# Performance work log

Hardware: AMD Instinct MI355X
Metric: run time of the kernel (lower is better)

The kernel has to match this reference:

```python
import jax, jax.numpy as jnp
import numpy as np

B_, L, D_MODEL = 2, 2048, 1024
EXPAND, D_INNER, D_STATE, DT_RANK, D_CONV = 2, 2048, 16, 64, 4
DT_MIN, DT_MAX = 0.001, 0.1


def setup_inputs() -> dict:
    key = jax.random.key(0)
    ks = jax.random.split(key, 8)
    s = lambda fan: 1.0 / np.sqrt(fan)
    # S4D-real style init for A: A = -exp(A_log), A_log = log(1..n) repeated over d_inner
    A0 = jnp.broadcast_to(jnp.arange(1, D_STATE + 1, dtype=jnp.float32), (D_INNER, D_STATE))
    return {
        "x": jax.random.normal(ks[0], (B_, L, D_MODEL), jnp.float32),
        "W_in": jax.random.normal(ks[1], (D_MODEL, 2 * D_INNER), jnp.float32) * s(D_MODEL),
        "conv_k": jax.random.normal(ks[2], (D_CONV, D_INNER // EXPAND, D_INNER), jnp.float32) * s(D_CONV * D_INNER // EXPAND),
        "conv_b": jnp.zeros((D_INNER,), jnp.float32),
        "W_x": jax.random.normal(ks[3], (D_INNER, DT_RANK + 2 * D_STATE), jnp.float32) * s(D_INNER),
        "W_dt": jax.random.normal(ks[4], (DT_RANK, D_INNER), jnp.float32) * s(DT_RANK),
        "b_dt": jnp.zeros((D_INNER,), jnp.float32),
        "A_log": jnp.log(A0),
        "D": jnp.ones((D_INNER,), jnp.float32),
        "W_out": jax.random.normal(ks[5], (D_INNER, D_MODEL), jnp.float32) * s(D_INNER),
    }


def reference(x, W_in, conv_k, conv_b, W_x, W_dt, b_dt, A_log, D, W_out):
    # in_proj -> split into ssm branch and gating residual branch
    xz = x @ W_in                                   # (b, l, 2*d_inner)
    xs, res = jnp.split(xz, 2, axis=-1)
    # causal grouped conv1d (feature_group_count = expand)
    xc = jax.lax.conv_general_dilated(
        xs, conv_k, window_strides=(1,), padding=[(D_CONV - 1, 0)],
        dimension_numbers=("NWC", "WIO", "NWC"), feature_group_count=EXPAND,
    ) + conv_b
    u = jax.nn.silu(xc)                             # (b, l, d_inner)
    # x_proj -> delta(low-rank), B, C
    dbc = u @ W_x                                   # (b, l, dt_rank + 2n)
    dt_raw = dbc[..., :DT_RANK]
    Bm = dbc[..., DT_RANK:DT_RANK + D_STATE]        # (b, l, n)
    Cm = dbc[..., DT_RANK + D_STATE:]               # (b, l, n)
    delta = jax.nn.softplus(dt_raw @ W_dt + b_dt)   # (b, l, d_inner)
    delta = jnp.clip(delta, DT_MIN, DT_MAX)
    A = -jnp.exp(A_log)                             # (d_inner, n)
    dA = jnp.exp(delta[..., None] * A)              # (b, l, d_inner, n)
    dBu = delta[..., None] * u[..., None] * Bm[:, :, None, :]  # (b, l, d_inner, n)

    def step(h, inp):
        dA_t, dBu_t, C_t = inp                      # (b,d,n),(b,d,n),(b,n)
        h = dA_t * h + dBu_t
        y_t = jnp.einsum('bdn,bn->bd', h, C_t)
        return h, y_t

    h0 = jnp.zeros((x.shape[0], D_INNER, D_STATE), dA.dtype)
    _, y = jax.lax.scan(step, h0, (dA.transpose(1, 0, 2, 3), dBu.transpose(1, 0, 2, 3), Cm.transpose(1, 0, 2)))
    y = y.transpose(1, 0, 2) + u * D                # (b, l, d_inner)
    out = (y * jax.nn.silu(res)) @ W_out            # (b, l, d_model)
    return out
```

## Files before the change

kernel.cpp:

```cpp
#include <hip/hip_runtime.h>
#include <math.h>


typedef unsigned short ushort_t;
typedef unsigned int uint_t;
typedef __bf16 bf16x8 __attribute__((ext_vector_type(8)));
typedef float floatx4 __attribute__((ext_vector_type(4)));

#define LDS_STRIDE 40

__device__ __forceinline__ float silu_f(float x) { return x / (1.0f + __expf(-x)); }

__device__ __forceinline__ unsigned short f2bf(float f) {
    unsigned u = __float_as_uint(f);
    unsigned r = u + 0x7fffu + ((u >> 16) & 1u);
    return (unsigned short)(r >> 16);
}
__device__ __forceinline__ float bf2f(unsigned short h) {
    return __uint_as_float(((unsigned)h) << 16);
}
__device__ __forceinline__ uint_t packhl(float v) {
    const unsigned short h = f2bf(v);
    const unsigned short l = f2bf(v - bf2f(h));
    return (uint_t)h | ((uint_t)l << 16);
}
__device__ __forceinline__ float unpack_sum(uint_t pk) {
    return __uint_as_float(pk << 16) + __uint_as_float(pk & 0xffff0000u);
}
__device__ __forceinline__ void unpack8(uint4 w0, uint4 w1, uint4& H, uint4& L) {
    H.x = (w0.x & 0xffffu) | (w0.y << 16);  L.x = (w0.x >> 16) | (w0.y & 0xffff0000u);
    H.y = (w0.z & 0xffffu) | (w0.w << 16);  L.y = (w0.z >> 16) | (w0.w & 0xffff0000u);
    H.z = (w1.x & 0xffffu) | (w1.y << 16);  L.z = (w1.x >> 16) | (w1.y & 0xffff0000u);
    H.w = (w1.z & 0xffffu) | (w1.w << 16);  L.w = (w1.z >> 16) | (w1.w & 0xffff0000u);
}

__global__ __launch_bounds__(256) void prep_all(
    const float* __restrict__ x, const float* __restrict__ W_in,
    const float* __restrict__ conv_k, const float* __restrict__ W_out,
    const float* __restrict__ W_x,
    uint_t* __restrict__ xpk,
    ushort_t* __restrict__ WinT_h, ushort_t* __restrict__ convkT_h,
    ushort_t* __restrict__ WoutT_h, ushort_t* __restrict__ WxT_h,
    ushort_t* __restrict__ XSP_h)
{
    __shared__ float ts[32][33];
    const int bid = blockIdx.x;
    const int t = threadIdx.x;
    if (bid < 4096) {
        const size_t i4 = ((size_t)bid * 256 + t) * 4;
        float4 v = *(const float4*)&x[i4];
        uint4 pk;
        pk.x = packhl(v.x); pk.y = packhl(v.y); pk.z = packhl(v.z); pk.w = packhl(v.w);
        *(uint4*)&xpk[i4] = pk;
        return;
    }
    if (bid >= 18432 && bid < 19456) {
        const int idx = (bid - 18432) * 256 + t;
        const int r = idx >> 11, k = idx & 2047;
        float v = (r < 96) ? W_x[(size_t)k * 96 + r] : 0.f;
        WxT_h[idx] = f2bf(v);
        return;
    }
    if (bid >= 19456) {
        const int idx = (bid - 19456) * 256 + t;
        const int b = idx / 6144, rem = idx % 6144;
        const int lp = rem >> 11, c = rem & 2047;
        XSP_h[((size_t)b * 2051 + lp) * 2048 + c] = 0;
        return;
    }
    const float* src; int R, C; ushort_t* dst; int bx, by;
    if (bid < 8192)       { src = W_in;   R = 1024; C = 4096; dst = WinT_h;
                            int l = bid - 4096;  bx = l & 127; by = l >> 7; }
    else if (bid < 16384) { src = conv_k; R = 4096; C = 2048; dst = convkT_h;
                            int l = bid - 8192;  bx = l & 63;  by = l >> 6; }
    else                  { src = W_out;  R = 2048; C = 1024; dst = WoutT_h;
                            int l = bid - 16384; bx = l & 31;  by = l >> 5; }
    const int tx = t & 31, ty = t >> 5;
    const int r0 = by * 32, c0 = bx * 32;
    #pragma unroll
    for (int j = 0; j < 4; ++j)
        ts[ty + j * 8][tx] = src[(size_t)(r0 + ty + j * 8) * C + c0 + tx];
    __syncthreads();
    #pragma unroll
    for (int j = 0; j < 4; ++j)
        dst[(size_t)(c0 + ty + j * 8) * R + r0 + tx] = f2bf(ts[tx][ty + j * 8]);
}

template<int MODE>
__global__ __launch_bounds__(256) void gemm2(
    const uint_t* __restrict__ Apk, const ushort_t* __restrict__ Bh, int Kfull,
    float* __restrict__ Cf, ushort_t* __restrict__ Oh)
{
    __shared__ __align__(16) ushort_t As_h[128 * LDS_STRIDE];
    __shared__ __align__(16) ushort_t As_l[128 * LDS_STRIDE];
    __shared__ __align__(16) ushort_t Bs_h[128 * LDS_STRIDE];
    const int t = threadIdx.x;
    int bx, by;
    if (MODE == 2) { bx = blockIdx.x; by = blockIdx.y; }
    else {
        const int lin = blockIdx.x, xcd = lin & 7, s = lin >> 3;
        bx = s >> 2;
        by = xcd * 4 + (s & 3);
    }
    const int m0 = by * 128;
    const int n0 = (MODE == 2) ? 0 : bx * 128;
    const int kbeg = (MODE == 2) ? bx * 512 : 0;
    const int kend = (MODE == 2) ? kbeg + 512 : Kfull;
    const int lane = t & 63, wave = t >> 6;
    const int wm = (wave >> 1) * 64, wn = (wave & 1) * 64;
    const int m16 = lane & 15, q = lane >> 4;
    const int r_0 = t >> 2, cc_0 = (t & 3) * 8;
    const int r_1 = (t + 256) >> 2, cc_1 = ((t + 256) & 3) * 8;

    uint4 a00 = *(const uint4*)&Apk[(size_t)(m0 + r_0) * Kfull + kbeg + cc_0];
    uint4 a01 = *(const uint4*)&Apk[(size_t)(m0 + r_0) * Kfull + kbeg + cc_0 + 4];
    uint4 a10 = *(const uint4*)&Apk[(size_t)(m0 + r_1) * Kfull + kbeg + cc_1];
    uint4 a11 = *(const uint4*)&Apk[(size_t)(m0 + r_1) * Kfull + kbeg + cc_1 + 4];
    uint4 pb0 = *(const uint4*)&Bh[(size_t)(n0 + r_0) * Kfull + kbeg + cc_0];
    uint4 pb1 = *(const uint4*)&Bh[(size_t)(n0 + r_1) * Kfull + kbeg + cc_1];

    floatx4 acc[4][4];
    const floatx4 zz = {0.f, 0.f, 0.f, 0.f};
    #pragma unroll
    for (int i = 0; i < 4; ++i)
        #pragma unroll
        for (int j = 0; j < 4; ++j) acc[i][j] = zz;

    for (int k0 = kbeg; k0 < kend; k0 += 32) {
        uint4 H, L;
        unpack8(a00, a01, H, L);
        *(uint4*)&As_h[r_0 * LDS_STRIDE + cc_0] = H;
        *(uint4*)&As_l[r_0 * LDS_STRIDE + cc_0] = L;
        unpack8(a10, a11, H, L);
        *(uint4*)&As_h[r_1 * LDS_STRIDE + cc_1] = H;
        *(uint4*)&As_l[r_1 * LDS_STRIDE + cc_1] = L;
        *(uint4*)&Bs_h[r_0 * LDS_STRIDE + cc_0] = pb0;
        *(uint4*)&Bs_h[r_1 * LDS_STRIDE + cc_1] = pb1;
        __syncthreads();
        if (k0 + 32 < kend) {
            const int kn = k0 + 32;
            a00 = *(const uint4*)&Apk[(size_t)(m0 + r_0) * Kfull + kn + cc_0];
            a01 = *(const uint4*)&Apk[(size_t)(m0 + r_0) * Kfull + kn + cc_0 + 4];
            a10 = *(const uint4*)&Apk[(size_t)(m0 + r_1) * Kfull + kn + cc_1];
            a11 = *(const uint4*)&Apk[(size_t)(m0 + r_1) * Kfull + kn + cc_1 + 4];
            pb0 = *(const uint4*)&Bh[(size_t)(n0 + r_0) * Kfull + kn + cc_0];
            pb1 = *(const uint4*)&Bh[(size_t)(n0 + r_1) * Kfull + kn + cc_1];
        }
        bf16x8 ah[4], al[4], bh[4];
        #pragma unroll
        for (int i = 0; i < 4; ++i) {
            const int off = (wm + i * 16 + m16) * LDS_STRIDE + q * 8;
            ah[i] = *(const bf16x8*)&As_h[off];
            al[i] = *(const bf16x8*)&As_l[off];
        }
        #pragma unroll
        for (int j = 0; j < 4; ++j)
            bh[j] = *(const bf16x8*)&Bs_h[(wn + j * 16 + m16) * LDS_STRIDE + q * 8];
        #pragma unroll
        for (int i = 0; i < 4; ++i)
            #pragma unroll
            for (int j = 0; j < 4; ++j) {
                acc[i][j] = __builtin_amdgcn_mfma_f32_16x16x32_bf16(ah[i], bh[j], acc[i][j], 0, 0, 0);
                acc[i][j] = __builtin_amdgcn_mfma_f32_16x16x32_bf16(al[i], bh[j], acc[i][j], 0, 0, 0);
            }
        __syncthreads();
    }

    float* Cp = (MODE == 2) ? (Cf + (size_t)bx * 393216) : Cf;
    #pragma unroll
    for (int i = 0; i < 4; ++i) {
        const int row_b = m0 + wm + i * 16 + q * 4;
        #pragma unroll
        for (int j = 0; j < 4; ++j) {
            const int col = n0 + wn + j * 16 + m16;
            #pragma unroll
            for (int rr = 0; rr < 4; ++rr) {
                const int row = row_b + rr;
                const float v = acc[i][j][rr];
                if (MODE == 0) {
                    if (n0 < 2048) {
                        const int b = row >> 11, l = row & 2047;
                        Oh[((size_t)b * 2051 + l + 3) * 2048 + col] = f2bf(v);
                    } else {
                        Cp[(size_t)row * 2048 + (col - 2048)] = v;
                    }
                } else if (MODE == 1) {
                    Cp[(size_t)row * 1024 + col] = v;
                } else {
                    if (col < 96) Cp[(size_t)row * 96 + col] = v;
                }
            }
        }
    }
}

__global__ __launch_bounds__(256) void conv2(
    const ushort_t* __restrict__ Xh, const ushort_t* __restrict__ Bh,
    const float* __restrict__ bias, uint_t* __restrict__ Upk)
{
    __shared__ __align__(16) ushort_t As_h[128 * LDS_STRIDE];
    __shared__ __align__(16) ushort_t Bs_h[128 * LDS_STRIDE];
    const int t = threadIdx.x;
    const int lin = blockIdx.x, xcd = lin & 7, s = lin >> 3;
    const int sweep = s >> 5, r = s & 31;
    const int bxp = r >> 1;
    const int by = xcd * 4 + ((sweep << 1) | (r & 1));
    const int m0 = by * 128, n0 = bxp * 128;
    const int g1024 = (n0 >= 1024) ? 1024 : 0;
    const int lane = t & 63, wave = t >> 6;
    const int wm = (wave >> 1) * 64, wn = (wave & 1) * 64;
    const int m16 = lane & 15, q = lane >> 4;
    const int r_0 = t >> 2, cc_0 = (t & 3) * 8;
    const int r_1 = (t + 256) >> 2, cc_1 = ((t + 256) & 3) * 8;
    const int p_0 = m0 + r_0, b_0 = p_0 >> 11, l_0 = p_0 & 2047;
    const int p_1 = m0 + r_1, b_1 = p_1 >> 11, l_1 = p_1 & 2047;

    auto aA = [&](int bb, int ll, int k0, int cc) -> size_t {
        const int w = k0 >> 10;
        const int i = (k0 & 1023) + cc;
        return ((size_t)bb * 2051 + ll + w) * 2048 + g1024 + i;
    };

    uint4 pa0 = *(const uint4*)&Xh[aA(b_0, l_0, 0, cc_0)];
    uint4 pa1 = *(const uint4*)&Xh[aA(b_1, l_1, 0, cc_1)];
    uint4 pb0 = *(const uint4*)&Bh[(size_t)(n0 + r_0) * 4096 + cc_0];
    uint4 pb1 = *(const uint4*)&Bh[(size_t)(n0 + r_1) * 4096 + cc_1];

    floatx4 acc[4][4];
    const floatx4 zz = {0.f, 0.f, 0.f, 0.f};
    #pragma unroll
    for (int i = 0; i < 4; ++i)
        #pragma unroll
        for (int j = 0; j < 4; ++j) acc[i][j] = zz;

    for (int k0 = 0; k0 < 4096; k0 += 32) {
        *(uint4*)&As_h[r_0 * LDS_STRIDE + cc_0] = pa0;
        *(uint4*)&As_h[r_1 * LDS_STRIDE + cc_1] = pa1;
        *(uint4*)&Bs_h[r_0 * LDS_STRIDE + cc_0] = pb0;
        *(uint4*)&Bs_h[r_1 * LDS_STRIDE + cc_1] = pb1;
        __syncthreads();
        if (k0 + 32 < 4096) {
            const int kn = k0 + 32;
            pa0 = *(const uint4*)&Xh[aA(b_0, l_0, kn, cc_0)];
            pa1 = *(const uint4*)&Xh[aA(b_1, l_1, kn, cc_1)];
            pb0 = *(const uint4*)&Bh[(size_t)(n0 + r_0) * 4096 + kn + cc_0];
            pb1 = *(const uint4*)&Bh[(size_t)(n0 + r_1) * 4096 + kn + cc_1];
        }
        bf16x8 ah[4], bh[4];
        #pragma unroll
        for (int i = 0; i < 4; ++i)
            ah[i] = *(const bf16x8*)&As_h[(wm + i * 16 + m16) * LDS_STRIDE + q * 8];
        #pragma unroll
        for (int j = 0; j < 4; ++j)
            bh[j] = *(const bf16x8*)&Bs_h[(wn + j * 16 + m16) * LDS_STRIDE + q * 8];
        #pragma unroll
        for (int i = 0; i < 4; ++i)
            #pragma unroll
            for (int j = 0; j < 4; ++j)
                acc[i][j] = __builtin_amdgcn_mfma_f32_16x16x32_bf16(ah[i], bh[j], acc[i][j], 0, 0, 0);
        __syncthreads();
    }

    #pragma unroll
    for (int i = 0; i < 4; ++i) {
        const int row_b = m0 + wm + i * 16 + q * 4;
        #pragma unroll
        for (int j = 0; j < 4; ++j) {
            const int col = n0 + wn + j * 16 + m16;
            const float bz = bias[col];
            #pragma unroll
            for (int rr = 0; rr < 4; ++rr) {
                const int row = row_b + rr;
                const float v = silu_f(acc[i][j][rr] + bz);
                Upk[(size_t)row * 2048 + col] = packhl(v);
            }
        }
    }
}

__global__ __launch_bounds__(256) void dbc_reduce(
    const float* __restrict__ DBCP, float* __restrict__ DBC)
{
    const int i = blockIdx.x * 256 + threadIdx.x;
    DBC[i] = (DBCP[i] + DBCP[393216 + i]) + (DBCP[786432 + i] + DBCP[1179648 + i]);
}

__global__ __launch_bounds__(256) void delta_kernel(
    const float* __restrict__ DBC, const float* __restrict__ W_dt,
    const float* __restrict__ b_dt, float* __restrict__ DELTA)
{
    const int n  = blockIdx.x * 256 + threadIdx.x;
    const int p0 = blockIdx.y * 16;
    const int t  = threadIdx.x;
    __shared__ float dt_s[16][64];
    #pragma unroll
    for (int j = 0; j < 4; ++j) {
        const int lin = j * 256 + t;
        const int r = lin >> 6, k = lin & 63;
        dt_s[r][k] = DBC[(size_t)(p0 + r) * 96 + k];
    }
    __syncthreads();
    float acc[16];
    const float bz = b_dt[n];
    #pragma unroll
    for (int r = 0; r < 16; ++r) acc[r] = bz;
    for (int k = 0; k < 64; ++k) {
        const float wv = W_dt[(size_t)k * 2048 + n];
        #pragma unroll
        for (int r = 0; r < 16; ++r) acc[r] += dt_s[r][k] * wv;
    }
    #pragma unroll
    for (int r = 0; r < 16; ++r) {
        float a = acc[r];
        float sp = (a > 20.f) ? a : log1pf(expf(a));
        sp = fminf(fmaxf(sp, 0.001f), 0.1f);
        DELTA[(size_t)(p0 + r) * 2048 + n] = sp;
    }
}

__global__ __launch_bounds__(256) void scan_p1(
    const float* __restrict__ DELTA, const uint_t* __restrict__ Upk,
    const float* __restrict__ DBC, const float* __restrict__ A_log,
    float* __restrict__ HEND, float* __restrict__ SD)
{
    const int t = threadIdx.x;
    const int d = blockIdx.x * 256 + t;
    const int c = blockIdx.y;
    const int b = blockIdx.z;
    const int p0 = b * 2048 + c * 32;
    __shared__ float Bs[32][16];
    for (int lin = t; lin < 512; lin += 256) {
        const int s = lin >> 4, n = lin & 15;
        Bs[s][n] = DBC[(size_t)(p0 + s) * 96 + 64 + n];
    }
    __syncthreads();
    float Af[16];
    *(float4*)&Af[0]  = *(const float4*)&A_log[(size_t)d * 16 + 0];
    *(float4*)&Af[4]  = *(const float4*)&A_log[(size_t)d * 16 + 4];
    *(float4*)&Af[8]  = *(const float4*)&A_log[(size_t)d * 16 + 8];
    *(float4*)&Af[12] = *(const float4*)&A_log[(size_t)d * 16 + 12];
    #pragma unroll
    for (int n = 0; n < 16; ++n) Af[n] = -__expf(Af[n]);

    float h[16] = {};
    float sd = 0.f;
    for (int s = 0; s < 32; ++s) {
        const size_t ix = (size_t)(p0 + s) * 2048 + d;
        const float dv = DELTA[ix];
        const float uv = unpack_sum(Upk[ix]);
        const float du = dv * uv;
        sd += dv;
        #pragma unroll
        for (int n = 0; n < 16; ++n)
            h[n] = __expf(dv * Af[n]) * h[n] + du * Bs[s][n];
    }
    const size_t hb = (((size_t)c * 2 + b) * 2048 + d) * 16;
    *(float4*)&HEND[hb + 0]  = *(float4*)&h[0];
    *(float4*)&HEND[hb + 4]  = *(float4*)&h[4];
    *(float4*)&HEND[hb + 8]  = *(float4*)&h[8];
    *(float4*)&HEND[hb + 12] = *(float4*)&h[12];
    SD[((size_t)c * 2 + b) * 2048 + d] = sd;
}

__global__ __launch_bounds__(256) void scan_p2(
    const float* __restrict__ HEND, const float* __restrict__ SD,
    const float* __restrict__ A_log, float* __restrict__ HINIT)
{
    const int g = blockIdx.x * 256 + threadIdx.x;
    const int n = g & 15, d = (g >> 4) & 2047, b = (g >> 15) & 1;
    const float Af = -__expf(A_log[(size_t)d * 16 + n]);
    float h = 0.f;
    #pragma unroll 8
    for (int c = 0; c < 64; ++c) {
        const size_t cb = (size_t)c * 2 + b;
        const size_t idx = (cb * 2048 + d) * 16 + n;
        HINIT[idx] = h;
        h = __expf(Af * SD[cb * 2048 + d]) * h + HEND[idx];
    }
}

__global__ __launch_bounds__(256) void scan_p3(
    const float* __restrict__ DELTA, const uint_t* __restrict__ Upk,
    const float* __restrict__ DBC, const float* __restrict__ RES,
    const float* __restrict__ A_log, const float* __restrict__ Dp,
    const float* __restrict__ HINIT, uint_t* __restrict__ Gpk)
{
    const int t = threadIdx.x;
    const int d = blockIdx.x * 256 + t;
    const int c = blockIdx.y;
    const int b = blockIdx.z;
    const int p0 = b * 2048 + c * 32;
    __shared__ float Bs[32][16];
    __shared__ float Cs[32][16];
    for (int lin = t; lin < 512; lin += 256) {
        const int s = lin >> 4, n = lin & 15;
        Bs[s][n] = DBC[(size_t)(p0 + s) * 96 + 64 + n];
        Cs[s][n] = DBC[(size_t)(p0 + s) * 96 + 80 + n];
    }
    __syncthreads();
    float Af[16];
    *(float4*)&Af[0]  = *(const float4*)&A_log[(size_t)d * 16 + 0];
    *(float4*)&Af[4]  = *(const float4*)&A_log[(size_t)d * 16 + 4];
    *(float4*)&Af[8]  = *(const float4*)&A_log[(size_t)d * 16 + 8];
    *(float4*)&Af[12] = *(const float4*)&A_log[(size_t)d * 16 + 12];
    #pragma unroll
    for (int n = 0; n < 16; ++n) Af[n] = -__expf(Af[n]);

    const size_t hb = (((size_t)c * 2 + b) * 2048 + d) * 16;
    float h[16];
    *(float4*)&h[0]  = *(const float4*)&HINIT[hb + 0];
    *(float4*)&h[4]  = *(const float4*)&HINIT[hb + 4];
    *(float4*)&h[8]  = *(const float4*)&HINIT[hb + 8];
    *(float4*)&h[12] = *(const float4*)&HINIT[hb + 12];
    const float Dd = Dp[d];

    for (int s = 0; s < 32; ++s) {
        const int p = p0 + s;
        const size_t ix = (size_t)p * 2048 + d;
        const float dv = DELTA[ix];
        const float uv = unpack_sum(Upk[ix]);
        const float du = dv * uv;
        float y = 0.f;
        #pragma unroll
        for (int n = 0; n < 16; ++n) {
            h[n] = __expf(dv * Af[n]) * h[n] + du * Bs[s][n];
            y += h[n] * Cs[s][n];
        }
        const float resv = RES[ix];
        const float gv = (y + uv * Dd) * silu_f(resv);
        Gpk[ix] = packhl(gv);
    }
}

extern "C" void kernel_launch(void* const* d_in, const int* in_sizes, int n_in,
                              void* d_out, int out_size, void* d_ws, size_t ws_size,
                              hipStream_t stream) {
    const float* x      = (const float*)d_in[0];
    const float* W_in   = (const float*)d_in[1];
    const float* conv_k = (const float*)d_in[2];
    const float* conv_b = (const float*)d_in[3];
    const float* W_x    = (const float*)d_in[4];
    const float* W_dt   = (const float*)d_in[5];
    const float* b_dt   = (const float*)d_in[6];
    const float* A_log  = (const float*)d_in[7];
    const float* Dv     = (const float*)d_in[8];
    const float* W_out  = (const float*)d_in[9];
    float* out = (float*)d_out;

    char* base = (char*)d_ws;
    float*    RES      = (float*)(base);
    uint_t*   Upk      = (uint_t*)(base + 33554432);
    float*    DELTA    = (float*)(base + 67108864);
    ushort_t* XSP_h    = (ushort_t*)(base + 100663296);
    float*    HEND     = (float*)(base + 100663296);
    uint_t*   xpk      = (uint_t*)(base + 117465088);
    ushort_t* convkT_h = (ushort_t*)(base + 134242304);
    uint_t*   Gpk      = (uint_t*)(base + 117465088);
    ushort_t* WinT_h   = (ushort_t*)(base + 151019520);
    ushort_t* WoutT_h  = (ushort_t*)(base + 159408128);
    ushort_t* WxT_h    = (ushort_t*)(base + 163602432);
    float*    DBCP     = (float*)(base + 164126720);
    float*    DBC      = (float*)(base + 170418176);
    float*    SD       = (float*)(base + 171991040);
    float*    HINIT    = (float*)(base + 173039616);

    prep_all<<<19504, 256, 0, stream>>>(x, W_in, conv_k, W_out, W_x,
                                        xpk, WinT_h, convkT_h, WoutT_h,
                                        WxT_h, XSP_h);
    gemm2<0><<<1024, 256, 0, stream>>>(xpk, WinT_h, 1024, RES, XSP_h);
    conv2<<<512, 256, 0, stream>>>(XSP_h, convkT_h, conv_b, Upk);
    gemm2<2><<<dim3(4, 32), 256, 0, stream>>>(Upk, WxT_h, 2048, DBCP, nullptr);
    dbc_reduce<<<1536, 256, 0, stream>>>(DBCP, DBC);
    delta_kernel<<<dim3(8, 256), 256, 0, stream>>>(DBC, W_dt, b_dt, DELTA);
    scan_p1<<<dim3(8, 64, 2), 256, 0, stream>>>(DELTA, Upk, DBC, A_log, HEND, SD);
    scan_p2<<<256, 256, 0, stream>>>(HEND, SD, A_log, HINIT);
    scan_p3<<<dim3(8, 64, 2), 256, 0, stream>>>(DELTA, Upk, DBC, RES, A_log, Dv,
                                                HINIT, Gpk);
    gemm2<1><<<256, 256, 0, stream>>>(Gpk, WoutT_h, 2048, out, nullptr);
}
```

Before: 494.3 us.

## Pre-swizzle weight matrices into MFMA fragment layout and load B directly to registers

Weight transposes in prep now write bf16 weights in a per-16-column, per-32-k fragment order that matches the MFMA B operand lane layout. The GEMM and conv kernels then load each wave's B fragments straight from global memory into registers with one 16-byte load per fragment, dropping the B shared-memory tile and its LDS writes and reads. The cost is that the two waves sharing a column half of the tile each fetch the same B data from global/L2 (no LDS sharing), and more registers are held for the prefetch.

```diff
diff --git a/kernel.cpp b/kernel.cpp
--- a/kernel.cpp
+++ b/kernel.cpp
@@ -33,14 +33,18 @@
     H.z = (w1.x & 0xffffu) | (w1.y << 16);  L.z = (w1.x >> 16) | (w1.y & 0xffff0000u);
     H.w = (w1.z & 0xffffu) | (w1.w << 16);  L.w = (w1.z >> 16) | (w1.w & 0xffff0000u);
 }
+__device__ __forceinline__ size_t faddr(int n, int k, int KC) {
+    return ((size_t)((n >> 4) * KC + (k >> 5)) * 64 + (n & 15) + (((k >> 3) & 3) << 4)) * 8
+           + (k & 7);
+}
 
 __global__ __launch_bounds__(256) void prep_all(
     const float* __restrict__ x, const float* __restrict__ W_in,
     const float* __restrict__ conv_k, const float* __restrict__ W_out,
     const float* __restrict__ W_x,
     uint_t* __restrict__ xpk,
-    ushort_t* __restrict__ WinT_h, ushort_t* __restrict__ convkT_h,
-    ushort_t* __restrict__ WoutT_h, ushort_t* __restrict__ WxT_h,
+    ushort_t* __restrict__ WinF, ushort_t* __restrict__ convkF,
+    ushort_t* __restrict__ WoutF, ushort_t* __restrict__ WxF,
     ushort_t* __restrict__ XSP_h)
 {
     __shared__ float ts[32][33];
@@ -58,7 +62,7 @@
         const int idx = (bid - 18432) * 256 + t;
         const int r = idx >> 11, k = idx & 2047;
         float v = (r < 96) ? W_x[(size_t)k * 96 + r] : 0.f;
-        WxT_h[idx] = f2bf(v);
+        WxF[faddr(r, k, 64)] = f2bf(v);
         return;
     }
     if (bid >= 19456) {
@@ -68,12 +72,12 @@
         XSP_h[((size_t)b * 2051 + lp) * 2048 + c] = 0;
         return;
     }
-    const float* src; int R, C; ushort_t* dst; int bx, by;
-    if (bid < 8192)       { src = W_in;   R = 1024; C = 4096; dst = WinT_h;
+    const float* src; int R, C, KC; ushort_t* dst; int bx, by;
+    if (bid < 8192)       { src = W_in;   R = 1024; C = 4096; KC = 32;  dst = WinF;
                             int l = bid - 4096;  bx = l & 127; by = l >> 7; }
-    else if (bid < 16384) { src = conv_k; R = 4096; C = 2048; dst = convkT_h;
+    else if (bid < 16384) { src = conv_k; R = 4096; C = 2048; KC = 128; dst = convkF;
                             int l = bid - 8192;  bx = l & 63;  by = l >> 6; }
-    else                  { src = W_out;  R = 2048; C = 1024; dst = WoutT_h;
+    else                  { src = W_out;  R = 2048; C = 1024; KC = 64;  dst = WoutF;
                             int l = bid - 16384; bx = l & 31;  by = l >> 5; }
     const int tx = t & 31, ty = t >> 5;
     const int r0 = by * 32, c0 = bx * 32;
@@ -82,18 +86,19 @@
         ts[ty + j * 8][tx] = src[(size_t)(r0 + ty + j * 8) * C + c0 + tx];
     __syncthreads();
     #pragma unroll
-    for (int j = 0; j < 4; ++j)
-        dst[(size_t)(c0 + ty + j * 8) * R + r0 + tx] = f2bf(ts[tx][ty + j * 8]);
+    for (int j = 0; j < 4; ++j) {
+        const int n = c0 + ty + j * 8, k = r0 + tx;
+        dst[faddr(n, k, KC)] = f2bf(ts[tx][ty + j * 8]);
+    }
 }
 
 template<int MODE>
 __global__ __launch_bounds__(256) void gemm2(
-    const uint_t* __restrict__ Apk, const ushort_t* __restrict__ Bh, int Kfull,
+    const uint_t* __restrict__ Apk, const ushort_t* __restrict__ Bf, int Kfull,
     float* __restrict__ Cf, ushort_t* __restrict__ Oh)
 {
     __shared__ __align__(16) ushort_t As_h[128 * LDS_STRIDE];
     __shared__ __align__(16) ushort_t As_l[128 * LDS_STRIDE];
-    __shared__ __align__(16) ushort_t Bs_h[128 * LDS_STRIDE];
     const int t = threadIdx.x;
     int bx, by;
     if (MODE == 2) { bx = blockIdx.x; by = blockIdx.y; }
@@ -106,9 +111,11 @@
     const int n0 = (MODE == 2) ? 0 : bx * 128;
     const int kbeg = (MODE == 2) ? bx * 512 : 0;
     const int kend = (MODE == 2) ? kbeg + 512 : Kfull;
+    const int KC = Kfull >> 5;
     const int lane = t & 63, wave = t >> 6;
     const int wm = (wave >> 1) * 64, wn = (wave & 1) * 64;
     const int m16 = lane & 15, q = lane >> 4;
+    const int n16b = (n0 + wn) >> 4;
     const int r_0 = t >> 2, cc_0 = (t & 3) * 8;
     const int r_1 = (t + 256) >> 2, cc_1 = ((t + 256) & 3) * 8;
 
@@ -116,8 +123,13 @@
     uint4 a01 = *(const uint4*)&Apk[(size_t)(m0 + r_0) * Kfull + kbeg + cc_0 + 4];
     uint4 a10 = *(const uint4*)&Apk[(size_t)(m0 + r_1) * Kfull + kbeg + cc_1];
     uint4 a11 = *(const uint4*)&Apk[(size_t)(m0 + r_1) * Kfull + kbeg + cc_1 + 4];
-    uint4 pb0 = *(const uint4*)&Bh[(size_t)(n0 + r_0) * Kfull + kbeg + cc_0];
-    uint4 pb1 = *(const uint4*)&Bh[(size_t)(n0 + r_1) * Kfull + kbeg + cc_1];
+    bf16x8 bc[4];
+    {
+        const int kc = kbeg >> 5;
+        #pragma unroll
+        for (int j = 0; j < 4; ++j)
+            bc[j] = *(const bf16x8*)&Bf[(((size_t)(n16b + j) * KC + kc) * 64 + lane) * 8];
+    }
 
     floatx4 acc[4][4];
     const floatx4 zz = {0.f, 0.f, 0.f, 0.f};
@@ -134,19 +146,19 @@
         unpack8(a10, a11, H, L);
         *(uint4*)&As_h[r_1 * LDS_STRIDE + cc_1] = H;
         *(uint4*)&As_l[r_1 * LDS_STRIDE + cc_1] = L;
-        *(uint4*)&Bs_h[r_0 * LDS_STRIDE + cc_0] = pb0;
-        *(uint4*)&Bs_h[r_1 * LDS_STRIDE + cc_1] = pb1;
         __syncthreads();
+        bf16x8 bn[4];
         if (k0 + 32 < kend) {
-            const int kn = k0 + 32;
+            const int kn = k0 + 32, kc = kn >> 5;
             a00 = *(const uint4*)&Apk[(size_t)(m0 + r_0) * Kfull + kn + cc_0];
             a01 = *(const uint4*)&Apk[(size_t)(m0 + r_0) * Kfull + kn + cc_0 + 4];
             a10 = *(const uint4*)&Apk[(size_t)(m0 + r_1) * Kfull + kn + cc_1];
             a11 = *(const uint4*)&Apk[(size_t)(m0 + r_1) * Kfull + kn + cc_1 + 4];
-            pb0 = *(const uint4*)&Bh[(size_t)(n0 + r_0) * Kfull + kn + cc_0];
-            pb1 = *(const uint4*)&Bh[(size_t)(n0 + r_1) * Kfull + kn + cc_1];
-        }
-        bf16x8 ah[4], al[4], bh[4];
+            #pragma unroll
+            for (int j = 0; j < 4; ++j)
+                bn[j] = *(const bf16x8*)&Bf[(((size_t)(n16b + j) * KC + kc) * 64 + lane) * 8];
+        }
+        bf16x8 ah[4], al[4];
         #pragma unroll
         for (int i = 0; i < 4; ++i) {
             const int off = (wm + i * 16 + m16) * LDS_STRIDE + q * 8;
@@ -154,15 +166,14 @@
             al[i] = *(const bf16x8*)&As_l[off];
         }
         #pragma unroll
-        for (int j = 0; j < 4; ++j)
-            bh[j] = *(const bf16x8*)&Bs_h[(wn + j * 16 + m16) * LDS_STRIDE + q * 8];
-        #pragma unroll
         for (int i = 0; i < 4; ++i)
             #pragma unroll
             for (int j = 0; j < 4; ++j) {
-                acc[i][j] = __builtin_amdgcn_mfma_f32_16x16x32_bf16(ah[i], bh[j], acc[i][j], 0, 0, 0);
-                acc[i][j] = __builtin_amdgcn_mfma_f32_16x16x32_bf16(al[i], bh[j], acc[i][j], 0, 0, 0);
+                acc[i][j] = __builtin_amdgcn_mfma_f32_16x16x32_bf16(ah[i], bc[j], acc[i][j], 0, 0, 0);
+                acc[i][j] = __builtin_amdgcn_mfma_f32_16x16x32_bf16(al[i], bc[j], acc[i][j], 0, 0, 0);
             }
+        #pragma unroll
+        for (int j = 0; j < 4; ++j) bc[j] = bn[j];
         __syncthreads();
     }
 
@@ -195,11 +206,10 @@
 }
 
 __global__ __launch_bounds__(256) void conv2(
-    const ushort_t* __restrict__ Xh, const ushort_t* __restrict__ Bh,
+    const ushort_t* __restrict__ Xh, const ushort_t* __restrict__ Bf,
     const float* __restrict__ bias, uint_t* __restrict__ Upk)
 {
     __shared__ __align__(16) ushort_t As_h[128 * LDS_STRIDE];
-    __shared__ __align__(16) ushort_t Bs_h[128 * LDS_STRIDE];
     const int t = threadIdx.x;
     const int lin = blockIdx.x, xcd = lin & 7, s = lin >> 3;
     const int sweep = s >> 5, r = s & 31;
@@ -210,6 +220,7 @@
     const int lane = t & 63, wave = t >> 6;
     const int wm = (wave >> 1) * 64, wn = (wave & 1) * 64;
     const int m16 = lane & 15, q = lane >> 4;
+    const int n16b = (n0 + wn) >> 4;
     const int r_0 = t >> 2, cc_0 = (t & 3) * 8;
     const int r_1 = (t + 256) >> 2, cc_1 = ((t + 256) & 3) * 8;
     const int p_0 = m0 + r_0, b_0 = p_0 >> 11, l_0 = p_0 & 2047;
@@ -223,8 +234,10 @@
 
     uint4 pa0 = *(const uint4*)&Xh[aA(b_0, l_0, 0, cc_0)];
     uint4 pa1 = *(const uint4*)&Xh[aA(b_1, l_1, 0, cc_1)];
-    uint4 pb0 = *(const uint4*)&Bh[(size_t)(n0 + r_0) * 4096 + cc_0];
-    uint4 pb1 = *(const uint4*)&Bh[(size_t)(n0 + r_1) * 4096 + cc_1];
+    bf16x8 bc[4];
+    #pragma unroll
+    for (int j = 0; j < 4; ++j)
+        bc[j] = *(const bf16x8*)&Bf[(((size_t)(n16b + j) * 128 + 0) * 64 + lane) * 8];
 
     floatx4 acc[4][4];
     const floatx4 zz = {0.f, 0.f, 0.f, 0.f};
@@ -236,28 +249,27 @@
     for (int k0 = 0; k0 < 4096; k0 += 32) {
         *(uint4*)&As_h[r_0 * LDS_STRIDE + cc_0] = pa0;
         *(uint4*)&As_h[r_1 * LDS_STRIDE + cc_1] = pa1;
-        *(uint4*)&Bs_h[r_0 * LDS_STRIDE + cc_0] = pb0;
-        *(uint4*)&Bs_h[r_1 * LDS_STRIDE + cc_1] = pb1;
         __syncthreads();
+        bf16x8 bn[4];
         if (k0 + 32 < 4096) {
-            const int kn = k0 + 32;
+            const int kn = k0 + 32, kc = kn >> 5;
             pa0 = *(const uint4*)&Xh[aA(b_0, l_0, kn, cc_0)];
             pa1 = *(const uint4*)&Xh[aA(b_1, l_1, kn, cc_1)];
-            pb0 = *(const uint4*)&Bh[(size_t)(n0 + r_0) * 4096 + kn + cc_0];
-            pb1 = *(const uint4*)&Bh[(size_t)(n0 + r_1) * 4096 + kn + cc_1];
-        }
-        bf16x8 ah[4], bh[4];
+            #pragma unroll
+            for (int j = 0; j < 4; ++j)
+                bn[j] = *(const bf16x8*)&Bf[(((size_t)(n16b + j) * 128 + kc) * 64 + lane) * 8];
+        }
+        bf16x8 ah[4];
         #pragma unroll
         for (int i = 0; i < 4; ++i)
             ah[i] = *(const bf16x8*)&As_h[(wm + i * 16 + m16) * LDS_STRIDE + q * 8];
         #pragma unroll
-        for (int j = 0; j < 4; ++j)
-            bh[j] = *(const bf16x8*)&Bs_h[(wn + j * 16 + m16) * LDS_STRIDE + q * 8];
-        #pragma unroll
         for (int i = 0; i < 4; ++i)
             #pragma unroll
             for (int j = 0; j < 4; ++j)
-                acc[i][j] = __builtin_amdgcn_mfma_f32_16x16x32_bf16(ah[i], bh[j], acc[i][j], 0, 0, 0);
+                acc[i][j] = __builtin_amdgcn_mfma_f32_16x16x32_bf16(ah[i], bc[j], acc[i][j], 0, 0, 0);
+        #pragma unroll
+        for (int j = 0; j < 4; ++j) bc[j] = bn[j];
         __syncthreads();
     }
 
@@ -454,27 +466,26 @@
     ushort_t* XSP_h    = (ushort_t*)(base + 100663296);
     float*    HEND     = (float*)(base + 100663296);
     uint_t*   xpk      = (uint_t*)(base + 117465088);
-    ushort_t* convkT_h = (ushort_t*)(base + 134242304);
+    ushort_t* convkF   = (ushort_t*)(base + 134242304);
     uint_t*   Gpk      = (uint_t*)(base + 117465088);
-    ushort_t* WinT_h   = (ushort_t*)(base + 151019520);
-    ushort_t* WoutT_h  = (ushort_t*)(base + 159408128);
-    ushort_t* WxT_h    = (ushort_t*)(base + 163602432);
+    ushort_t* WinF     = (ushort_t*)(base + 151019520);
+    ushort_t* WoutF    = (ushort_t*)(base + 159408128);
+    ushort_t* WxF      = (ushort_t*)(base + 163602432);
     float*    DBCP     = (float*)(base + 164126720);
     float*    DBC      = (float*)(base + 170418176);
     float*    SD       = (float*)(base + 171991040);
     float*    HINIT    = (float*)(base + 173039616);
 
     prep_all<<<19504, 256, 0, stream>>>(x, W_in, conv_k, W_out, W_x,
-                                        xpk, WinT_h, convkT_h, WoutT_h,
-                                        WxT_h, XSP_h);
-    gemm2<0><<<1024, 256, 0, stream>>>(xpk, WinT_h, 1024, RES, XSP_h);
-    conv2<<<512, 256, 0, stream>>>(XSP_h, convkT_h, conv_b, Upk);
-    gemm2<2><<<dim3(4, 32), 256, 0, stream>>>(Upk, WxT_h, 2048, DBCP, nullptr);
+                                        xpk, WinF, convkF, WoutF, WxF, XSP_h);
+    gemm2<0><<<1024, 256, 0, stream>>>(xpk, WinF, 1024, RES, XSP_h);
+    conv2<<<512, 256, 0, stream>>>(XSP_h, convkF, conv_b, Upk);
+    gemm2<2><<<dim3(4, 32), 256, 0, stream>>>(Upk, WxF, 2048, DBCP, nullptr);
     dbc_reduce<<<1536, 256, 0, stream>>>(DBCP, DBC);
     delta_kernel<<<dim3(8, 256), 256, 0, stream>>>(DBC, W_dt, b_dt, DELTA);
     scan_p1<<<dim3(8, 64, 2), 256, 0, stream>>>(DELTA, Upk, DBC, A_log, HEND, SD);
     scan_p2<<<256, 256, 0, stream>>>(HEND, SD, A_log, HINIT);
     scan_p3<<<dim3(8, 64, 2), 256, 0, stream>>>(DELTA, Upk, DBC, RES, A_log, Dv,
                                                 HINIT, Gpk);
-    gemm2<1><<<256, 256, 0, stream>>>(Gpk, WoutT_h, 2048, out, nullptr);
-}
+    gemm2<1><<<256, 256, 0, stream>>>(Gpk, WoutF, 2048, out, nullptr);
+}
```

Result: no change. 491.5 us (-0.6%).
